# Kernel optimization log

Hardware: AMD Instinct MI355X
Metric: run time of the kernel (lower is better)

## Reference

```python
import jax, jax.numpy as jnp
import numpy as np

N, M, D = 8192, 65536, 512

def setup_inputs() -> dict:
    key = jax.random.key(0)
    k1, k2 = jax.random.split(key)
    embedding = jax.random.normal(k1, (N, D), dtype=jnp.float32)
    memory_bank = jax.random.normal(k2, (M, D), dtype=jnp.float32)
    return {"embedding": embedding, "memory_bank": memory_bank}

def reference(embedding, memory_bank):
    # torch.cdist(embedding, memory_bank, p=2.0) via the expansion
    x_sq = jnp.sum(embedding * embedding, axis=1, keepdims=True)        # [N, 1]
    m_sq = jnp.sum(memory_bank * memory_bank, axis=1)[None, :]          # [1, M]
    cross = embedding @ memory_bank.T                                    # [N, M]
    dist_sq = jnp.maximum(x_sq + m_sq - 2.0 * cross, 0.0)
    distances = jnp.sqrt(dist_sq)                                        # [N, M]
    # distances.topk(k=1, largest=False, dim=1) -> per-row min, kept dim
    patch_scores = jnp.min(distances, axis=1, keepdims=True)             # [N, 1]
    return patch_scores
```

## Files before the change

### kernel.cpp

```cpp
#include <hip/hip_runtime.h>
#include <stdint.h>

#define NROWS 8192
#define MROWS 65536
#define DDIM  512
#define BK    64
#define CT_PER_BLOCK 16
#define NBLOCKS 2048

typedef __attribute__((ext_vector_type(4))) float f32x4;
typedef __attribute__((ext_vector_type(8))) short short8;
typedef unsigned short ushort_t;
typedef unsigned int   uint_t;

__device__ __forceinline__ ushort_t f2bf(float x) {
    uint_t u = __float_as_uint(x);
    u += 0x7fffu + ((u >> 16) & 1u);
    return (ushort_t)(u >> 16);
}
__device__ __forceinline__ float bf2f(ushort_t b) {
    return __uint_as_float(((uint_t)b) << 16);
}

__device__ __forceinline__ void gll16(const void* g, void* l) {
    __builtin_amdgcn_global_load_lds((__attribute__((address_space(1))) void*)g,
                                     (__attribute__((address_space(3))) void*)l,
                                     16, 0, 0);
}

__global__ void init_minsq(uint_t* minsq) {
    int i = blockIdx.x * 256 + threadIdx.x;
    if (i < NROWS) minsq[i] = 0x7f800000u;
}

__global__ void norms_kernel(const float* __restrict__ emb, const float* __restrict__ mem,
                             float* __restrict__ xsq, float* __restrict__ msq) {
    int row  = blockIdx.x * 4 + (threadIdx.x >> 6);
    int lane = threadIdx.x & 63;
    const float* src;
    float* dst;
    if (row < NROWS) { src = emb + (size_t)row * DDIM;           dst = xsq + row; }
    else             { src = mem + (size_t)(row - NROWS) * DDIM; dst = msq + (row - NROWS); }
    float4 f0 = *(const float4*)(src + lane * 8);
    float4 f1 = *(const float4*)(src + lane * 8 + 4);
    float s = 0.f, v;
    v = bf2f(f2bf(f0.x)); s += v * v;
    v = bf2f(f2bf(f0.y)); s += v * v;
    v = bf2f(f2bf(f0.z)); s += v * v;
    v = bf2f(f2bf(f0.w)); s += v * v;
    v = bf2f(f2bf(f1.x)); s += v * v;
    v = bf2f(f2bf(f1.y)); s += v * v;
    v = bf2f(f2bf(f1.z)); s += v * v;
    v = bf2f(f2bf(f1.w)); s += v * v;
    #pragma unroll
    for (int o = 1; o < 64; o <<= 1) s += __shfl_xor(s, o);
    if (lane == 0) *dst = s;
}

__global__ void convert_kernel(const float* __restrict__ emb, const float* __restrict__ mem,
                               ushort_t* __restrict__ Abf, ushort_t* __restrict__ Bbf) {
    unsigned gid = blockIdx.x * 256 + threadIdx.x;
    unsigned row = gid >> 6;
    unsigned within = gid & 63u;
    unsigned seg = within >> 3, cc = within & 7u;
    const float* src; ushort_t* dst; unsigned r;
    if (row < NROWS) { r = row;         src = emb + (size_t)r * DDIM; dst = Abf + (size_t)r * DDIM; }
    else             { r = row - NROWS; src = mem + (size_t)r * DDIM; dst = Bbf + (size_t)r * DDIM; }
    unsigned scc = cc ^ (r & 7u);
    const float4* s4 = (const float4*)(src + seg * 64 + scc * 8);
    float4 a = s4[0], b = s4[1];
    uint4 w;
    w.x = (uint_t)f2bf(a.x) | ((uint_t)f2bf(a.y) << 16);
    w.y = (uint_t)f2bf(a.z) | ((uint_t)f2bf(a.w) << 16);
    w.z = (uint_t)f2bf(b.x) | ((uint_t)f2bf(b.y) << 16);
    w.w = (uint_t)f2bf(b.z) | ((uint_t)f2bf(b.w) << 16);
    *(uint4*)(dst + seg * 64 + cc * 8) = w;
}

__device__ __forceinline__ void stage_load(const float* __restrict__ emb,
                                           const float* __restrict__ mem,
                                           size_t r0, size_t c0, int ks,
                                           float4* ra, float4* rb, int tid) {
    #pragma unroll
    for (int p = 0; p < 4; ++p) {
        int row = p * 32 + (tid >> 3);
        int c   = (tid & 7) * 8;
        const float* sa = emb + (r0 + row) * DDIM + ks * BK + c;
        const float* sb = mem + (c0 + row) * DDIM + ks * BK + c;
        ra[2*p]   = *(const float4*)sa;
        ra[2*p+1] = *(const float4*)(sa + 4);
        rb[2*p]   = *(const float4*)sb;
        rb[2*p+1] = *(const float4*)(sb + 4);
    }
}

__device__ __forceinline__ void stage_write(ushort_t* Ab, ushort_t* Bb,
                                            const float4* ra, const float4* rb, int tid) {
    #pragma unroll
    for (int p = 0; p < 4; ++p) {
        int row = p * 32 + (tid >> 3);
        int ccs = (tid & 7) ^ (row & 7);
        uint4 wa, wb;
        wa.x = (uint_t)f2bf(ra[2*p].x)   | ((uint_t)f2bf(ra[2*p].y)   << 16);
        wa.y = (uint_t)f2bf(ra[2*p].z)   | ((uint_t)f2bf(ra[2*p].w)   << 16);
        wa.z = (uint_t)f2bf(ra[2*p+1].x) | ((uint_t)f2bf(ra[2*p+1].y) << 16);
        wa.w = (uint_t)f2bf(ra[2*p+1].z) | ((uint_t)f2bf(ra[2*p+1].w) << 16);
        wb.x = (uint_t)f2bf(rb[2*p].x)   | ((uint_t)f2bf(rb[2*p].y)   << 16);
        wb.y = (uint_t)f2bf(rb[2*p].z)   | ((uint_t)f2bf(rb[2*p].w)   << 16);
        wb.z = (uint_t)f2bf(rb[2*p+1].x) | ((uint_t)f2bf(rb[2*p+1].y) << 16);
        wb.w = (uint_t)f2bf(rb[2*p+1].z) | ((uint_t)f2bf(rb[2*p+1].w) << 16);
        *(uint4*)&Ab[row * BK + ccs * 8] = wa;
        *(uint4*)&Bb[row * BK + ccs * 8] = wb;
    }
}

template<bool PRECONV>
__global__ __launch_bounds__(256, 2) void gemm_min_kernel(
    const float* __restrict__ emb, const float* __restrict__ mem,
    const ushort_t* __restrict__ Abf, const ushort_t* __restrict__ Bbf,
    const float* __restrict__ xsq, const float* __restrict__ msq,
    uint_t* __restrict__ minsq)
{
    __shared__ alignas(16) ushort_t Ab[128 * BK];
    __shared__ alignas(16) ushort_t Bb[128 * BK];

    const int tid  = threadIdx.x;
    const int lane = tid & 63;
    const int wave = tid >> 6;
    const int wm = wave >> 1, wn = wave & 1;

    unsigned wg  = blockIdx.x;
    unsigned swz = (wg & 7u) * (NBLOCKS / 8) + (wg >> 3);
    const unsigned rt = swz & 63u;
    const unsigned cg = swz >> 6;
    const size_t r0 = (size_t)rt * 128;

    float runmin[4][4];
    #pragma unroll
    for (int m = 0; m < 4; ++m)
        #pragma unroll
        for (int j = 0; j < 4; ++j) runmin[m][j] = 3.0e38f;

    float4 ra[8], rb[8];

    for (int ct = 0; ct < CT_PER_BLOCK; ++ct) {
        const size_t c0 = ((size_t)cg * CT_PER_BLOCK + ct) * 128;

        f32x4 acc[4][4] = {};

        if constexpr (!PRECONV) {
            stage_load(emb, mem, r0, c0, 0, ra, rb, tid);
        }

        for (int ks = 0; ks < DDIM / BK; ++ks) {
            if constexpr (PRECONV) {
                #pragma unroll
                for (int i = 0; i < 4; ++i) {
                    int t     = (i * 4 + wave) * 1024 + lane * 16;
                    int rowi  = t >> 7;
                    int inrow = t & 127;
                    const char* gA = (const char*)Abf + (r0 + rowi) * 1024 + (size_t)ks * 128 + inrow;
                    const char* gB = (const char*)Bbf + (c0 + rowi) * 1024 + (size_t)ks * 128 + inrow;
                    gll16(gA, (char*)Ab + (i * 4 + wave) * 1024);
                    gll16(gB, (char*)Bb + (i * 4 + wave) * 1024);
                }
                __syncthreads();
            } else {
                __syncthreads();
                stage_write(Ab, Bb, ra, rb, tid);
                if (ks + 1 < DDIM / BK) stage_load(emb, mem, r0, c0, ks + 1, ra, rb, tid);
                __syncthreads();
            }

            #pragma unroll
            for (int kk = 0; kk < 2; ++kk) {
                short8 af[4], bfm[4];
                #pragma unroll
                for (int m = 0; m < 4; ++m) {
                    int r = wm * 64 + m * 16 + (lane & 15);
                    int c = ((kk * 4 + (lane >> 4)) ^ (r & 7)) * 8;
                    af[m] = *(const short8*)&Ab[r * BK + c];
                }
                #pragma unroll
                for (int n = 0; n < 4; ++n) {
                    int r = wn * 64 + n * 16 + (lane & 15);
                    int c = ((kk * 4 + (lane >> 4)) ^ (r & 7)) * 8;
                    bfm[n] = *(const short8*)&Bb[r * BK + c];
                }
                #pragma unroll
                for (int m = 0; m < 4; ++m)
                    #pragma unroll
                    for (int n = 0; n < 4; ++n)
                        acc[m][n] = __builtin_amdgcn_mfma_f32_16x16x32_bf16(af[m], bfm[n], acc[m][n], 0, 0, 0);
            }
            if constexpr (PRECONV) __syncthreads();
        }

        float mc[4];
        #pragma unroll
        for (int n = 0; n < 4; ++n) mc[n] = msq[c0 + wn * 64 + n * 16 + (lane & 15)];
        #pragma unroll
        for (int m = 0; m < 4; ++m)
            #pragma unroll
            for (int n = 0; n < 4; ++n)
                #pragma unroll
                for (int j = 0; j < 4; ++j)
                    runmin[m][j] = fminf(runmin[m][j], fmaf(-2.f, acc[m][n][j], mc[n]));
    }

    #pragma unroll
    for (int m = 0; m < 4; ++m)
        #pragma unroll
        for (int j = 0; j < 4; ++j) {
            float v = runmin[m][j];
            v = fminf(v, __shfl_xor(v, 1));
            v = fminf(v, __shfl_xor(v, 2));
            v = fminf(v, __shfl_xor(v, 4));
            v = fminf(v, __shfl_xor(v, 8));
            if ((lane & 15) == 0) {
                int grow = (int)r0 + wm * 64 + m * 16 + (lane >> 4) * 4 + j;
                float d2 = fmaxf(v + xsq[grow], 0.f);
                atomicMin(&minsq[grow], __float_as_uint(d2));
            }
        }
}

__global__ void finish_kernel(const uint_t* __restrict__ minsq, float* __restrict__ out) {
    int i = blockIdx.x * 256 + threadIdx.x;
    if (i < NROWS) out[i] = sqrtf(__uint_as_float(minsq[i]));
}

extern "C" void kernel_launch(void* const* d_in, const int* in_sizes, int n_in,
                              void* d_out, int out_size, void* d_ws, size_t ws_size,
                              hipStream_t stream) {
    const float* emb = (const float*)d_in[0];
    const float* mem = (const float*)d_in[1];
    float* out = (float*)d_out;

    char* ws = (char*)d_ws;
    float*  xsq   = (float*)ws;
    float*  msq   = (float*)(ws + 32768);
    uint_t* minsq = (uint_t*)(ws + 32768 + 262144);
    ushort_t* Abf = (ushort_t*)(ws + 327680);
    ushort_t* Bbf = Abf + (size_t)NROWS * DDIM;
    const size_t NEED = 327680 + ((size_t)NROWS + MROWS) * DDIM * 2;

    init_minsq<<<(NROWS + 255) / 256, 256, 0, stream>>>(minsq);
    norms_kernel<<<(NROWS + MROWS) / 4, 256, 0, stream>>>(emb, mem, xsq, msq);
    if (ws_size >= NEED) {
        convert_kernel<<<((NROWS + MROWS) * 64) / 256, 256, 0, stream>>>(emb, mem, Abf, Bbf);
        gemm_min_kernel<true><<<NBLOCKS, 256, 0, stream>>>(emb, mem, Abf, Bbf, xsq, msq, minsq);
    } else {
        gemm_min_kernel<false><<<NBLOCKS, 256, 0, stream>>>(emb, mem, Abf, Bbf, xsq, msq, minsq);
    }
    finish_kernel<<<(NROWS + 255) / 256, 256, 0, stream>>>(minsq, out);
}
```

Baseline: 616.3 us.

## Use 256x256 double-buffered bf16 GEMM tiles and fuse norms into conversion

Replaces the 128x128 pre-converted GEMM with a 512-thread kernel that computes 256x256 tiles with BK=32. Global-to-LDS loads are double-buffered and interleaved with MFMA half-steps, using explicit barriers, waitcnts and setprio. The row-norm computation is folded into the bf16 conversion kernel so the inputs are read once less. The larger tiles raise arithmetic intensity but need many more registers, which risks occupancy and spills, and the hand-written scheduling is fragile.

```diff
diff --git a/kernel.cpp b/kernel.cpp
--- a/kernel.cpp
+++ b/kernel.cpp
@@ -4,9 +4,14 @@
 #define NROWS 8192
 #define MROWS 65536
 #define DDIM  512
-#define BK    64
-#define CT_PER_BLOCK 16
-#define NBLOCKS 2048
+
+#define BM 256
+#define BN 256
+#define BKK 32
+#define CT 8
+#define KT_PER_CT (DDIM / BKK)
+#define NT (CT * KT_PER_CT)
+#define GRID_X ((NROWS / BM) * (MROWS / (BN * CT)))
 
 typedef __attribute__((ext_vector_type(4))) float f32x4;
 typedef __attribute__((ext_vector_type(8))) short short8;
@@ -28,74 +33,223 @@
                                      16, 0, 0);
 }
 
+#define SBAR()  __builtin_amdgcn_s_barrier()
+#define SCHED0() __builtin_amdgcn_sched_barrier(0)
+
 __global__ void init_minsq(uint_t* minsq) {
     int i = blockIdx.x * 256 + threadIdx.x;
     if (i < NROWS) minsq[i] = 0x7f800000u;
+}
+
+__global__ void convert_norms(const float* __restrict__ emb, const float* __restrict__ mem,
+                              ushort_t* __restrict__ Abf, ushort_t* __restrict__ Bbf,
+                              float* __restrict__ xsq, float* __restrict__ msq) {
+    unsigned gid = blockIdx.x * 256 + threadIdx.x;
+    unsigned row = gid >> 6;
+    unsigned within = gid & 63u;
+    unsigned seg = within >> 2, cc = within & 3u;
+    int lane = threadIdx.x & 63;
+    const float* src; ushort_t* dst; float* nrm; unsigned r;
+    if (row < NROWS) { r = row;         src = emb + (size_t)r * DDIM; dst = Abf + (size_t)r * DDIM; nrm = xsq + r; }
+    else             { r = row - NROWS; src = mem + (size_t)r * DDIM; dst = Bbf + (size_t)r * DDIM; nrm = msq + r; }
+    unsigned scc = cc ^ ((r >> 1) & 3u);
+    const float4* s4 = (const float4*)(src + seg * 32 + scc * 8);
+    float4 a = s4[0], b = s4[1];
+    ushort_t q[8];
+    q[0]=f2bf(a.x); q[1]=f2bf(a.y); q[2]=f2bf(a.z); q[3]=f2bf(a.w);
+    q[4]=f2bf(b.x); q[5]=f2bf(b.y); q[6]=f2bf(b.z); q[7]=f2bf(b.w);
+    uint4 w;
+    w.x = (uint_t)q[0] | ((uint_t)q[1] << 16);
+    w.y = (uint_t)q[2] | ((uint_t)q[3] << 16);
+    w.z = (uint_t)q[4] | ((uint_t)q[5] << 16);
+    w.w = (uint_t)q[6] | ((uint_t)q[7] << 16);
+    *(uint4*)(dst + seg * 32 + cc * 8) = w;
+    float s = 0.f;
+    #pragma unroll
+    for (int i = 0; i < 8; ++i) { float v = bf2f(q[i]); s += v * v; }
+    #pragma unroll
+    for (int o = 1; o < 64; o <<= 1) s += __shfl_xor(s, o);
+    if (lane == 0) *nrm = s;
+}
+
+__global__ __launch_bounds__(512, 2) void gemm256_min(
+    const ushort_t* __restrict__ Abf, const ushort_t* __restrict__ Bbf,
+    const float* __restrict__ xsq, const float* __restrict__ msq,
+    uint_t* __restrict__ minsq)
+{
+    __shared__ alignas(16) ushort_t As[2][BM * BKK];
+    __shared__ alignas(16) ushort_t Bs[2][BN * BKK];
+
+    const int tid  = threadIdx.x;
+    const int lane = tid & 63;
+    const int wave = tid >> 6;
+    const int wm   = wave >> 2;
+    const int wn   = wave & 3;
+    const int laneRow = lane & 15;
+    const int laneK   = lane >> 4;
+
+    unsigned wg  = blockIdx.x;
+    unsigned swz = (wg & 7u) * (GRID_X / 8) + (wg >> 3);
+    const unsigned rt = swz & 31u;
+    const unsigned cg = swz >> 5;
+    const size_t r0    = (size_t)rt * BM;
+    const size_t cbase = (size_t)cg * (BN * CT);
+
+    const int chunk = ((laneK ^ ((laneRow >> 1) & 3)) << 4);
+    int offA[8], offB[4];
+    #pragma unroll
+    for (int m = 0; m < 8; ++m) offA[m] = (wm * 128 + m * 16 + laneRow) * 64 + chunk;
+    #pragma unroll
+    for (int n = 0; n < 4; ++n) offB[n] = (wn * 64 + n * 16 + laneRow) * 64 + chunk;
+
+    const int rowoff = wave * 16 + (lane >> 2);
+    const int inrow  = (lane & 3) * 16;
+    const char* Ag = (const char*)Abf + (r0 + rowoff) * 1024 + inrow;
+
+    f32x4 acc[8][4];
+    float runmin[8][4];
+    #pragma unroll
+    for (int m = 0; m < 8; ++m)
+        #pragma unroll
+        for (int n = 0; n < 4; ++n) { acc[m][n] = (f32x4)0.f; runmin[m][n] = 3.0e38f; }
+
+    {
+        const char* Asrc = Ag;
+        const char* Bsrc = (const char*)Bbf + (cbase + rowoff) * 1024 + inrow;
+        char* Ad = (char*)&As[0][0] + wave * 1024;
+        char* Bd = (char*)&Bs[0][0] + wave * 1024;
+        gll16(Asrc, Ad);                     gll16(Bsrc, Bd);
+        gll16(Asrc + 131072, Ad + 8192);     gll16(Bsrc + 131072, Bd + 8192);
+        asm volatile("s_waitcnt vmcnt(0)" ::: "memory");
+        SCHED0(); SBAR(); SCHED0();
+    }
+
+    for (int t = 0; t < NT; ++t) {
+        const int cur = t & 1;
+        const char* AbC = (const char*)&As[cur][0];
+        const char* BbC = (const char*)&Bs[cur][0];
+        const bool stg = (t + 1) < NT;
+        const char* AsrcN = nullptr; const char* BsrcN = nullptr;
+        char* AdN = nullptr; char* BdN = nullptr;
+        if (stg) {
+            int t2 = t + 1;
+            int ks2 = t2 & 15, ct2 = t2 >> 4;
+            AsrcN = Ag + (size_t)ks2 * 64;
+            BsrcN = (const char*)Bbf + (cbase + (size_t)ct2 * BN + rowoff) * 1024 + inrow + (size_t)ks2 * 64;
+            AdN = (char*)&As[cur ^ 1][0] + wave * 1024;
+            BdN = (char*)&Bs[cur ^ 1][0] + wave * 1024;
+        }
+
+        short8 af[4], bfr[4];
+        #pragma unroll
+        for (int m = 0; m < 4; ++m) af[m]  = *(const short8*)(AbC + offA[m]);
+        #pragma unroll
+        for (int n = 0; n < 4; ++n) bfr[n] = *(const short8*)(BbC + offB[n]);
+        if (stg) { gll16(AsrcN, AdN); gll16(BsrcN, BdN); }
+        SCHED0(); SBAR(); SCHED0();
+        asm volatile("s_waitcnt lgkmcnt(0)" ::: "memory");
+        SCHED0();
+        __builtin_amdgcn_s_setprio(1);
+        #pragma unroll
+        for (int m = 0; m < 4; ++m)
+            #pragma unroll
+            for (int n = 0; n < 4; ++n)
+                acc[m][n] = __builtin_amdgcn_mfma_f32_16x16x32_bf16(af[m], bfr[n], acc[m][n], 0, 0, 0);
+        __builtin_amdgcn_s_setprio(0);
+        SCHED0(); SBAR(); SCHED0();
+
+        short8 ag[4];
+        #pragma unroll
+        for (int m = 0; m < 4; ++m) ag[m] = *(const short8*)(AbC + offA[m + 4]);
+        if (stg) { gll16(AsrcN + 131072, AdN + 8192); gll16(BsrcN + 131072, BdN + 8192); }
+        SCHED0(); SBAR(); SCHED0();
+        asm volatile("s_waitcnt lgkmcnt(0)" ::: "memory");
+        SCHED0();
+        __builtin_amdgcn_s_setprio(1);
+        #pragma unroll
+        for (int m = 0; m < 4; ++m)
+            #pragma unroll
+            for (int n = 0; n < 4; ++n)
+                acc[m + 4][n] = __builtin_amdgcn_mfma_f32_16x16x32_bf16(ag[m], bfr[n], acc[m + 4][n], 0, 0, 0);
+        __builtin_amdgcn_s_setprio(0);
+        SCHED0();
+        asm volatile("s_waitcnt vmcnt(0)" ::: "memory");
+        SCHED0(); SBAR(); SCHED0();
+
+        if ((t & 15) == 15) {
+            const size_t c0 = cbase + (size_t)(t >> 4) * BN;
+            float mc[4];
+            #pragma unroll
+            for (int n = 0; n < 4; ++n) mc[n] = msq[c0 + wn * 64 + n * 16 + laneRow];
+            #pragma unroll
+            for (int m = 0; m < 8; ++m)
+                #pragma unroll
+                for (int n = 0; n < 4; ++n) {
+                    #pragma unroll
+                    for (int j = 0; j < 4; ++j)
+                        runmin[m][j] = fminf(runmin[m][j], fmaf(-2.f, acc[m][n][j], mc[n]));
+                    acc[m][n] = (f32x4)0.f;
+                }
+        }
+    }
+
+    #pragma unroll
+    for (int m = 0; m < 8; ++m)
+        #pragma unroll
+        for (int j = 0; j < 4; ++j) {
+            float v = runmin[m][j];
+            v = fminf(v, __shfl_xor(v, 1));
+            v = fminf(v, __shfl_xor(v, 2));
+            v = fminf(v, __shfl_xor(v, 4));
+            v = fminf(v, __shfl_xor(v, 8));
+            if ((lane & 15) == 0) {
+                int grow = (int)r0 + wm * 128 + m * 16 + laneK * 4 + j;
+                float d2 = fmaxf(v + xsq[grow], 0.f);
+                atomicMin(&minsq[grow], __float_as_uint(d2));
+            }
+        }
+}
+
+__global__ void finish_kernel(const uint_t* __restrict__ minsq, float* __restrict__ out) {
+    int i = blockIdx.x * 256 + threadIdx.x;
+    if (i < NROWS) out[i] = sqrtf(__uint_as_float(minsq[i]));
 }
 
 __global__ void norms_kernel(const float* __restrict__ emb, const float* __restrict__ mem,
                              float* __restrict__ xsq, float* __restrict__ msq) {
     int row  = blockIdx.x * 4 + (threadIdx.x >> 6);
     int lane = threadIdx.x & 63;
-    const float* src;
-    float* dst;
+    const float* src; float* dst;
     if (row < NROWS) { src = emb + (size_t)row * DDIM;           dst = xsq + row; }
     else             { src = mem + (size_t)(row - NROWS) * DDIM; dst = msq + (row - NROWS); }
     float4 f0 = *(const float4*)(src + lane * 8);
     float4 f1 = *(const float4*)(src + lane * 8 + 4);
     float s = 0.f, v;
-    v = bf2f(f2bf(f0.x)); s += v * v;
-    v = bf2f(f2bf(f0.y)); s += v * v;
-    v = bf2f(f2bf(f0.z)); s += v * v;
-    v = bf2f(f2bf(f0.w)); s += v * v;
-    v = bf2f(f2bf(f1.x)); s += v * v;
-    v = bf2f(f2bf(f1.y)); s += v * v;
-    v = bf2f(f2bf(f1.z)); s += v * v;
-    v = bf2f(f2bf(f1.w)); s += v * v;
+    v = bf2f(f2bf(f0.x)); s += v*v;  v = bf2f(f2bf(f0.y)); s += v*v;
+    v = bf2f(f2bf(f0.z)); s += v*v;  v = bf2f(f2bf(f0.w)); s += v*v;
+    v = bf2f(f2bf(f1.x)); s += v*v;  v = bf2f(f2bf(f1.y)); s += v*v;
+    v = bf2f(f2bf(f1.z)); s += v*v;  v = bf2f(f2bf(f1.w)); s += v*v;
     #pragma unroll
     for (int o = 1; o < 64; o <<= 1) s += __shfl_xor(s, o);
     if (lane == 0) *dst = s;
 }
 
-__global__ void convert_kernel(const float* __restrict__ emb, const float* __restrict__ mem,
-                               ushort_t* __restrict__ Abf, ushort_t* __restrict__ Bbf) {
-    unsigned gid = blockIdx.x * 256 + threadIdx.x;
-    unsigned row = gid >> 6;
-    unsigned within = gid & 63u;
-    unsigned seg = within >> 3, cc = within & 7u;
-    const float* src; ushort_t* dst; unsigned r;
-    if (row < NROWS) { r = row;         src = emb + (size_t)r * DDIM; dst = Abf + (size_t)r * DDIM; }
-    else             { r = row - NROWS; src = mem + (size_t)r * DDIM; dst = Bbf + (size_t)r * DDIM; }
-    unsigned scc = cc ^ (r & 7u);
-    const float4* s4 = (const float4*)(src + seg * 64 + scc * 8);
-    float4 a = s4[0], b = s4[1];
-    uint4 w;
-    w.x = (uint_t)f2bf(a.x) | ((uint_t)f2bf(a.y) << 16);
-    w.y = (uint_t)f2bf(a.z) | ((uint_t)f2bf(a.w) << 16);
-    w.z = (uint_t)f2bf(b.x) | ((uint_t)f2bf(b.y) << 16);
-    w.w = (uint_t)f2bf(b.z) | ((uint_t)f2bf(b.w) << 16);
-    *(uint4*)(dst + seg * 64 + cc * 8) = w;
-}
-
-__device__ __forceinline__ void stage_load(const float* __restrict__ emb,
-                                           const float* __restrict__ mem,
-                                           size_t r0, size_t c0, int ks,
-                                           float4* ra, float4* rb, int tid) {
+__device__ __forceinline__ void fb_stage_load(const float* __restrict__ emb,
+                                              const float* __restrict__ mem,
+                                              size_t r0, size_t c0, int ks,
+                                              float4* ra, float4* rb, int tid) {
     #pragma unroll
     for (int p = 0; p < 4; ++p) {
         int row = p * 32 + (tid >> 3);
         int c   = (tid & 7) * 8;
-        const float* sa = emb + (r0 + row) * DDIM + ks * BK + c;
-        const float* sb = mem + (c0 + row) * DDIM + ks * BK + c;
-        ra[2*p]   = *(const float4*)sa;
-        ra[2*p+1] = *(const float4*)(sa + 4);
-        rb[2*p]   = *(const float4*)sb;
-        rb[2*p+1] = *(const float4*)(sb + 4);
-    }
-}
-
-__device__ __forceinline__ void stage_write(ushort_t* Ab, ushort_t* Bb,
-                                            const float4* ra, const float4* rb, int tid) {
+        const float* sa = emb + (r0 + row) * DDIM + ks * 64 + c;
+        const float* sb = mem + (c0 + row) * DDIM + ks * 64 + c;
+        ra[2*p]   = *(const float4*)sa;  ra[2*p+1] = *(const float4*)(sa + 4);
+        rb[2*p]   = *(const float4*)sb;  rb[2*p+1] = *(const float4*)(sb + 4);
+    }
+}
+__device__ __forceinline__ void fb_stage_write(ushort_t* Ab, ushort_t* Bb,
+                                               const float4* ra, const float4* rb, int tid) {
     #pragma unroll
     for (int p = 0; p < 4; ++p) {
         int row = p * 32 + (tid >> 3);
@@ -109,69 +263,39 @@
         wb.y = (uint_t)f2bf(rb[2*p].z)   | ((uint_t)f2bf(rb[2*p].w)   << 16);
         wb.z = (uint_t)f2bf(rb[2*p+1].x) | ((uint_t)f2bf(rb[2*p+1].y) << 16);
         wb.w = (uint_t)f2bf(rb[2*p+1].z) | ((uint_t)f2bf(rb[2*p+1].w) << 16);
-        *(uint4*)&Ab[row * BK + ccs * 8] = wa;
-        *(uint4*)&Bb[row * BK + ccs * 8] = wb;
-    }
-}
-
-template<bool PRECONV>
-__global__ __launch_bounds__(256, 2) void gemm_min_kernel(
+        *(uint4*)&Ab[row * 64 + ccs * 8] = wa;
+        *(uint4*)&Bb[row * 64 + ccs * 8] = wb;
+    }
+}
+
+__global__ __launch_bounds__(256, 2) void gemm_min_fb(
     const float* __restrict__ emb, const float* __restrict__ mem,
-    const ushort_t* __restrict__ Abf, const ushort_t* __restrict__ Bbf,
     const float* __restrict__ xsq, const float* __restrict__ msq,
     uint_t* __restrict__ minsq)
 {
-    __shared__ alignas(16) ushort_t Ab[128 * BK];
-    __shared__ alignas(16) ushort_t Bb[128 * BK];
-
-    const int tid  = threadIdx.x;
-    const int lane = tid & 63;
-    const int wave = tid >> 6;
+    __shared__ alignas(16) ushort_t Ab[128 * 64];
+    __shared__ alignas(16) ushort_t Bb[128 * 64];
+    const int tid = threadIdx.x, lane = tid & 63, wave = tid >> 6;
     const int wm = wave >> 1, wn = wave & 1;
-
-    unsigned wg  = blockIdx.x;
-    unsigned swz = (wg & 7u) * (NBLOCKS / 8) + (wg >> 3);
-    const unsigned rt = swz & 63u;
-    const unsigned cg = swz >> 6;
+    unsigned wg = blockIdx.x;
+    unsigned swz = (wg & 7u) * (2048 / 8) + (wg >> 3);
+    const unsigned rt = swz & 63u, cgf = swz >> 6;
     const size_t r0 = (size_t)rt * 128;
-
     float runmin[4][4];
     #pragma unroll
     for (int m = 0; m < 4; ++m)
         #pragma unroll
         for (int j = 0; j < 4; ++j) runmin[m][j] = 3.0e38f;
-
     float4 ra[8], rb[8];
-
-    for (int ct = 0; ct < CT_PER_BLOCK; ++ct) {
-        const size_t c0 = ((size_t)cg * CT_PER_BLOCK + ct) * 128;
-
+    for (int ctf = 0; ctf < 16; ++ctf) {
+        const size_t c0 = ((size_t)cgf * 16 + ctf) * 128;
         f32x4 acc[4][4] = {};
-
-        if constexpr (!PRECONV) {
-            stage_load(emb, mem, r0, c0, 0, ra, rb, tid);
-        }
-
-        for (int ks = 0; ks < DDIM / BK; ++ks) {
-            if constexpr (PRECONV) {
-                #pragma unroll
-                for (int i = 0; i < 4; ++i) {
-                    int t     = (i * 4 + wave) * 1024 + lane * 16;
-                    int rowi  = t >> 7;
-                    int inrow = t & 127;
-                    const char* gA = (const char*)Abf + (r0 + rowi) * 1024 + (size_t)ks * 128 + inrow;
-                    const char* gB = (const char*)Bbf + (c0 + rowi) * 1024 + (size_t)ks * 128 + inrow;
-                    gll16(gA, (char*)Ab + (i * 4 + wave) * 1024);
-                    gll16(gB, (char*)Bb + (i * 4 + wave) * 1024);
-                }
-                __syncthreads();
-            } else {
-                __syncthreads();
-                stage_write(Ab, Bb, ra, rb, tid);
-                if (ks + 1 < DDIM / BK) stage_load(emb, mem, r0, c0, ks + 1, ra, rb, tid);
-                __syncthreads();
-            }
-
+        fb_stage_load(emb, mem, r0, c0, 0, ra, rb, tid);
+        for (int ks = 0; ks < 8; ++ks) {
+            __syncthreads();
+            fb_stage_write(Ab, Bb, ra, rb, tid);
+            if (ks + 1 < 8) fb_stage_load(emb, mem, r0, c0, ks + 1, ra, rb, tid);
+            __syncthreads();
             #pragma unroll
             for (int kk = 0; kk < 2; ++kk) {
                 short8 af[4], bfm[4];
@@ -179,13 +303,13 @@
                 for (int m = 0; m < 4; ++m) {
                     int r = wm * 64 + m * 16 + (lane & 15);
                     int c = ((kk * 4 + (lane >> 4)) ^ (r & 7)) * 8;
-                    af[m] = *(const short8*)&Ab[r * BK + c];
+                    af[m] = *(const short8*)&Ab[r * 64 + c];
                 }
                 #pragma unroll
                 for (int n = 0; n < 4; ++n) {
                     int r = wn * 64 + n * 16 + (lane & 15);
                     int c = ((kk * 4 + (lane >> 4)) ^ (r & 7)) * 8;
-                    bfm[n] = *(const short8*)&Bb[r * BK + c];
+                    bfm[n] = *(const short8*)&Bb[r * 64 + c];
                 }
                 #pragma unroll
                 for (int m = 0; m < 4; ++m)
@@ -193,9 +317,7 @@
                     for (int n = 0; n < 4; ++n)
                         acc[m][n] = __builtin_amdgcn_mfma_f32_16x16x32_bf16(af[m], bfm[n], acc[m][n], 0, 0, 0);
             }
-            if constexpr (PRECONV) __syncthreads();
-        }
-
+        }
         float mc[4];
         #pragma unroll
         for (int n = 0; n < 4; ++n) mc[n] = msq[c0 + wn * 64 + n * 16 + (lane & 15)];
@@ -207,7 +329,6 @@
                 for (int j = 0; j < 4; ++j)
                     runmin[m][j] = fminf(runmin[m][j], fmaf(-2.f, acc[m][n][j], mc[n]));
     }
-
     #pragma unroll
     for (int m = 0; m < 4; ++m)
         #pragma unroll
@@ -225,11 +346,6 @@
         }
 }
 
-__global__ void finish_kernel(const uint_t* __restrict__ minsq, float* __restrict__ out) {
-    int i = blockIdx.x * 256 + threadIdx.x;
-    if (i < NROWS) out[i] = sqrtf(__uint_as_float(minsq[i]));
-}
-
 extern "C" void kernel_launch(void* const* d_in, const int* in_sizes, int n_in,
                               void* d_out, int out_size, void* d_ws, size_t ws_size,
                               hipStream_t stream) {
@@ -246,12 +362,12 @@
     const size_t NEED = 327680 + ((size_t)NROWS + MROWS) * DDIM * 2;
 
     init_minsq<<<(NROWS + 255) / 256, 256, 0, stream>>>(minsq);
-    norms_kernel<<<(NROWS + MROWS) / 4, 256, 0, stream>>>(emb, mem, xsq, msq);
     if (ws_size >= NEED) {
-        convert_kernel<<<((NROWS + MROWS) * 64) / 256, 256, 0, stream>>>(emb, mem, Abf, Bbf);
-        gemm_min_kernel<true><<<NBLOCKS, 256, 0, stream>>>(emb, mem, Abf, Bbf, xsq, msq, minsq);
+        convert_norms<<<((NROWS + MROWS) * 64) / 256, 256, 0, stream>>>(emb, mem, Abf, Bbf, xsq, msq);
+        gemm256_min<<<GRID_X, 512, 0, stream>>>(Abf, Bbf, xsq, msq, minsq);
     } else {
-        gemm_min_kernel<false><<<NBLOCKS, 256, 0, stream>>>(emb, mem, Abf, Bbf, xsq, msq, minsq);
+        norms_kernel<<<(NROWS + MROWS) / 4, 256, 0, stream>>>(emb, mem, xsq, msq);
+        gemm_min_fb<<<2048, 256, 0, stream>>>(emb, mem, xsq, msq, minsq);
     }
     finish_kernel<<<(NROWS + 255) / 256, 256, 0, stream>>>(minsq, out);
 }
```

Measured after the change: 593.7 us. 1.04x faster.
